# Optimization experiments

Hardware: AMD Instinct MI355X
Metric: run time of the kernel (lower is better)

## Reference

```python
import jax, jax.numpy as jnp
import numpy as np

N = 10000      # nodes
E = 160000     # edges
MUL = 64       # multiplicity of 0e and 1o in node feats / target
NATTR = 10     # number of element types (node_attrs one-hot width)
RDIM = 8       # radial (edge_feats) dim
NAVG = 16.0    # num_avg_neighbors
_INV3 = 0.5773502691896258  # CG coeff for 1o x 1o -> 0e (1/sqrt(3))


def setup_inputs() -> dict:
    key = jax.random.key(0)
    ks = jax.random.split(key, 20)
    return {
        "node_attrs": jax.random.uniform(ks[0], (N, NATTR), jnp.float32),
        "node_feats": jax.random.normal(ks[1], (N, 4 * MUL), jnp.float32),
        "edge_attrs_real": jax.random.normal(ks[2], (E, 4), jnp.float32),
        "edge_attrs_imag": jax.random.normal(ks[3], (E, 4), jnp.float32),
        "edge_feats": jax.random.normal(ks[4], (E, RDIM), jnp.float32),
        # linear_up (per-l internal weights)
        "W_up0": jax.random.normal(ks[5], (MUL, MUL), jnp.float32),
        "W_up1": jax.random.normal(ks[6], (MUL, MUL), jnp.float32),
        # conv_tp_weights MLP: [8, 64, 64, 64, 4*MUL]
        "M1": jax.random.normal(ks[7], (RDIM, 64), jnp.float32),
        "M2": jax.random.normal(ks[8], (64, 64), jnp.float32),
        "M3": jax.random.normal(ks[9], (64, 64), jnp.float32),
        "M4": jax.random.normal(ks[10], (64, 4 * MUL), jnp.float32),
        # linear: irreps_mid (128x0e+128x1o) -> irreps_nonlin (128x0e+64x1o)
        "W_lin_s": jax.random.normal(ks[11], (2 * MUL, 2 * MUL), jnp.float32),
        "W_lin_v": jax.random.normal(ks[12], (2 * MUL, MUL), jnp.float32),
        # skip_tp: FullyConnectedTensorProduct(node_feats, node_attrs -> irreps_nonlin)
        "W_sk_s": jax.random.normal(ks[13], (MUL, NATTR, 2 * MUL), jnp.float32),
        "W_sk_v": jax.random.normal(ks[14], (MUL, NATTR, MUL), jnp.float32),
        "edge_index": jax.random.randint(ks[15], (2, E), 0, N, jnp.int64
                                         if jax.config.jax_enable_x64 else jnp.int32),
    }


def _forward(node_attrs, node_feats, edge_attrs_real, edge_attrs_imag, edge_feats,
             W_up0, W_up1, M1, M2, M3, M4, W_lin_s, W_lin_v, W_sk_s, W_sk_v,
             sender, receiver):
    n = node_feats.shape[0]
    x0 = node_feats[:, :MUL]                          # (N, 64)   64x0e
    x1 = node_feats[:, MUL:].reshape(n, MUL, 3)       # (N, 64, 3) 64x1o

    # skip TP (fully connected, node_attrs are scalars)
    sk_norm = 1.0 / np.sqrt(MUL * NATTR)
    sc_s = jnp.einsum('nu,na,uav->nv', x0, node_attrs, W_sk_s) * sk_norm   # (N,128)
    sc_v = jnp.einsum('nui,na,uav->nvi', x1, node_attrs, W_sk_v) * sk_norm # (N,64,3)

    # linear_up (per-l)
    up_norm = 1.0 / np.sqrt(MUL)
    x0 = (x0 @ W_up0) * up_norm
    x1 = jnp.einsum('nui,uv->nvi', x1, W_up1) * up_norm

    # radial MLP -> per-edge TP weights (4 uvu paths x MUL)
    h = jax.nn.silu((edge_feats @ M1) / np.sqrt(RDIM))
    h = jax.nn.silu((h @ M2) / 8.0)
    h = jax.nn.silu((h @ M3) / 8.0)
    tw = (h @ M4) / 8.0                               # (E, 256)
    wA, wB, wC, wD = (tw[:, :MUL], tw[:, MUL:2*MUL],
                      tw[:, 2*MUL:3*MUL], tw[:, 3*MUL:])

    xs0 = x0[sender]                                  # (E, 64)
    xs1 = x1[sender]                                  # (E, 64, 3)

    def conv_tp(y):
        # y: (E,4) = [0e | 1o]; uvu paths with per-edge weights
        y0, y1 = y[:, :1], y[:, 1:]
        s = jnp.concatenate([xs0 * y0 * wA,                                  # 0e x 0e -> 0e
                             jnp.einsum('eui,ei->eu', xs1, y1) * _INV3 * wD  # 1o x 1o -> 0e
                             ], axis=1)                                      # (E,128)
        v = jnp.concatenate([(xs0 * wB)[:, :, None] * y1[:, None, :],        # 0e x 1o -> 1o
                             xs1 * (y0 * wC)[:, :, None]                     # 1o x 0e -> 1o
                             ], axis=1)                                      # (E,128,3)
        return s, v

    sr, vr = conv_tp(edge_attrs_real)
    si, vi = conv_tp(edge_attrs_imag)

    ms_r = jax.ops.segment_sum(sr, receiver, num_segments=n)
    mv_r = jax.ops.segment_sum(vr, receiver, num_segments=n)
    ms_i = jax.ops.segment_sum(si, receiver, num_segments=n)
    mv_i = jax.ops.segment_sum(vi, receiver, num_segments=n)

    lin_norm = (1.0 / np.sqrt(2 * MUL)) / (2.0 * NAVG)

    def lin(ms, mv):
        return (ms @ W_lin_s) * lin_norm, jnp.einsum('nui,uv->nvi', mv, W_lin_v) * lin_norm

    def gate(s, v):
        # irreps_nonlin = 64x0e scalars | 64x0e gates | 64x1o gated
        scal = jax.nn.silu(s[:, :MUL])
        g = jax.nn.silu(s[:, MUL:])
        return jnp.concatenate([scal, (v * g[:, :, None]).reshape(n, 3 * MUL)], axis=1)

    ls, lv = lin(ms_r, mv_r)
    real = gate(ls + sc_s, lv + sc_v)                 # (N, 256), residual on real part
    lsi, lvi = lin(ms_i, mv_i)
    imag = gate(lsi, lvi)                             # (N, 256)

    # view_as_complex + reshape [N, num_features, dim//num_features]; complex kept
    # as trailing real/imag axis of size 2.
    return jnp.stack([real, imag], axis=-1).reshape(n, MUL, (4 * MUL) // MUL, 2)


def reference(node_attrs, node_feats, edge_attrs_real, edge_attrs_imag, edge_feats,
              W_up0, W_up1, M1, M2, M3, M4, W_lin_s, W_lin_v, W_sk_s, W_sk_v,
              edge_index):
    sender, receiver = edge_index[0], edge_index[1]
    return _forward(node_attrs, node_feats, edge_attrs_real, edge_attrs_imag,
                    edge_feats, W_up0, W_up1, M1, M2, M3, M4,
                    W_lin_s, W_lin_v, W_sk_s, W_sk_v, sender, receiver)
```

## Files before the change

kernel.cpp:

```cpp
#include <hip/hip_runtime.h>
#include <hip/hip_bf16.h>

#define NN 10000
#define NE 160000
#define NGRP 625
#define XPLN 640000

#define SK_NORM   0.039528470752104741f
#define UP_NORM   0.125f
#define M1_NORM   0.35355339059327373f
#define INV3      0.5773502691896258f
#define LIN_NORM  0.0027621358640099516f

__device__ __forceinline__ float siluf(float x) { return x / (1.0f + __expf(-x)); }

__device__ __forceinline__ unsigned short f2bf_bits(float x) {
    union { __hip_bfloat16 h; unsigned short u; } cv;
    cv.h = __float2bfloat16(x);
    return cv.u;
}
__device__ __forceinline__ float bflo(unsigned int w) { return __uint_as_float(w << 16); }
__device__ __forceinline__ float bfhi(unsigned int w) { return __uint_as_float(w & 0xffff0000u); }

typedef short bf16x8 __attribute__((ext_vector_type(8)));
typedef float f32x4  __attribute__((ext_vector_type(4)));

__global__ __launch_bounds__(256) void k_detect(const int* __restrict__ ei32, int* __restrict__ flag) {
    __shared__ int cnt;
    if (threadIdx.x == 0) cnt = 0;
    __syncthreads();
    int z = 0;
    for (int i = threadIdx.x; i < 1024; i += 256)
        if (ei32[2 * i + 1] == 0) z++;
    atomicAdd(&cnt, z);
    __syncthreads();
    if (threadIdx.x == 0) flag[0] = (cnt >= 512) ? 1 : 0;
}

__global__ __launch_bounds__(256) void k_cvt(const int* __restrict__ ei32, const int* __restrict__ flag,
                                             int* __restrict__ snd, int* __restrict__ rcv) {
    int e = blockIdx.x * 256 + threadIdx.x;
    if (e >= NE) return;
    if (flag[0]) {
        const long long* e64 = (const long long*)ei32;
        snd[e] = (int)e64[e];
        rcv[e] = (int)e64[NE + e];
    } else {
        snd[e] = ei32[e];
        rcv[e] = ei32[NE + e];
    }
}

__global__ __launch_bounds__(256) void k_wprepN(
    const float* __restrict__ Wsk_s, const float* __restrict__ Wsk_v,
    const float* __restrict__ Wu0, const float* __restrict__ Wu1,
    unsigned short* __restrict__ WNF) {
    int idx = blockIdx.x * 256 + threadIdx.x;
    if (idx >= 131072) return;
    float val;
    if (idx < 81920) {
        int p = idx / 10240, r = idx % 10240;
        int kc = r >> 9, l8 = r & 511;
        int lane = l8 >> 3, j = l8 & 7, quad = lane >> 4, lo = lane & 15;
        int a = kc >> 1, u = (kc & 1) * 32 + quad * 8 + j;
        val = Wsk_s[(u * 10 + a) * 128 + p * 16 + lo];
    } else if (idx < 122880) {
        int rel = idx - 81920;
        int p = rel / 10240, r = rel % 10240;
        int kc = r >> 9, l8 = r & 511;
        int lane = l8 >> 3, j = l8 & 7, quad = lane >> 4, lo = lane & 15;
        int a = kc >> 1, u = (kc & 1) * 32 + quad * 8 + j;
        val = Wsk_v[(u * 10 + a) * 64 + p * 16 + lo];
    } else if (idx < 126976) {
        int rel = idx - 122880;
        int p = rel >> 10, r = rel & 1023;
        int kc = r >> 9, l8 = r & 511;
        int lane = l8 >> 3, j = l8 & 7, quad = lane >> 4, lo = lane & 15;
        int u = kc * 32 + quad * 8 + j;
        val = Wu0[u * 64 + p * 16 + lo];
    } else {
        int rel = idx - 126976;
        int p = rel >> 10, r = rel & 1023;
        int kc = r >> 9, l8 = r & 511;
        int lane = l8 >> 3, j = l8 & 7, quad = lane >> 4, lo = lane & 15;
        int u = kc * 32 + quad * 8 + j;
        val = Wu1[u * 64 + p * 16 + lo];
    }
    WNF[idx] = f2bf_bits(val);
}

__global__ __launch_bounds__(256) void k_xprep(
    const float* __restrict__ node_attrs, const float* __restrict__ node_feats,
    unsigned short* __restrict__ xpk, float* __restrict__ attrsP) {
    int idx = blockIdx.x * 256 + threadIdx.x;
    if (idx < 4 * NN * 64) {
        int n = idx >> 8, c = idx & 255;
        int plane = c >> 6, u = c & 63;
        float v = (plane == 0) ? node_feats[(long)n * 256 + u]
                               : node_feats[(long)n * 256 + 64 + u * 3 + (plane - 1)];
        xpk[(size_t)plane * XPLN + (long)n * 64 + u] = f2bf_bits(v);
        return;
    }
    int i2 = idx - 4 * NN * 64;
    if (i2 < 10 * NN) {
        int a = i2 / NN, n = i2 - a * NN;
        attrsP[i2] = node_attrs[(long)n * 10 + a];
    }
}

__global__ __launch_bounds__(256) void k_wprep2(
    const float* __restrict__ M1, const float* __restrict__ M2,
    const float* __restrict__ M3, const float* __restrict__ M4,
    unsigned short* __restrict__ WFG) {
    int idx = blockIdx.x * 256 + threadIdx.x;
    if (idx >= 52 * 512) return;
    int f = idx >> 9, r = idx & 511;
    int lane = r >> 3, j = r & 7;
    int quad = lane >> 4, lo = lane & 15;
    float val;
    if (f < 4) {
        int n = f * 16 + lo, k = quad * 8 + j;
        val = (k < 8) ? M1[k * 64 + n] : 0.f;
    } else if (f < 12) {
        int g2 = f - 4, nt = g2 >> 1, half = g2 & 1;
        int n = nt * 16 + lo, k = half * 32 + quad * 8 + j;
        val = M2[k * 64 + n];
    } else if (f < 20) {
        int g3 = f - 12, nt = g3 >> 1, half = g3 & 1;
        int n = nt * 16 + lo, k = half * 32 + quad * 8 + j;
        val = M3[k * 64 + n];
    } else {
        int g4 = f - 20, tt = g4 >> 1, half = g4 & 1;
        int n = tt * 16 + lo, k = half * 32 + quad * 8 + j;
        val = M4[k * 256 + n];
    }
    WFG[idx] = f2bf_bits(val);
}

#define G0 8
#define NB0 79
#define G2 4
#define NB2 157
#define G3 16
#define NB3 40
#define KNODE_GRID (4*NB0 + 2*NB2 + 2*NB3)

__global__ __launch_bounds__(128) void k_node(
    const unsigned short* __restrict__ xpk, const float* __restrict__ attrsP,
    const unsigned short* __restrict__ WNF,
    float* __restrict__ sc_s, float* __restrict__ sc_v,
    float* __restrict__ x0u, float* __restrict__ x1p) {
    __shared__ unsigned short pan[2 * 10240];
    __shared__ float att[10 * 128];

    int t = threadIdx.x;
    int bid = blockIdx.x;
    int type, vp, chunk;
    if (bid < 4 * NB0)                 { type = 0; vp = bid / NB0; chunk = bid % NB0; }
    else if (bid < 4 * NB0 + 2 * NB2)  { int r = bid - 4 * NB0; type = 2; vp = r / NB2; chunk = r % NB2; }
    else                               { int r = bid - 4 * NB0 - 2 * NB2; type = 3; vp = r / NB3; chunk = r % NB3; }
    int G = (type == 0) ? G0 : (type == 2 ? G2 : G3);
    int g0 = chunk * G;
    int ng = NGRP - g0; if (ng > G) ng = G;
    int n0 = g0 * 16;

    int psrc, pcnt;
    if (type == 0)      { psrc = vp * 2 * 10240;           pcnt = 20480; }
    else if (type == 2) { psrc = 81920 + vp * 2 * 10240;   pcnt = 20480; }
    else                { psrc = 122880 + vp * 2 * 1024;   pcnt = 2048;  }
    for (int i = t; i < pcnt / 8; i += 128)
        ((float4*)pan)[i] = ((const float4*)(WNF + psrc))[i];
    if (type == 3) {
        for (int i = t; i < 2048 / 8; i += 128)
            ((float4*)(pan + 2048))[i] = ((const float4*)(WNF + 126976 + vp * 2 * 1024))[i];
    }
    if (type <= 2) {
        int cnt = ng * 16;
        #pragma unroll
        for (int k = 0; k < 10; k++) {
            int i = k * 128 + t;
            int nl = t;
            if (nl < cnt) att[i] = attrsP[k * NN + n0 + nl];
        }
    }
    __syncthreads();

    int wv = t >> 6, lane = t & 63, lo = lane & 15, quad = lane >> 4;
    int lbase = lane * 8;
    const f32x4 zacc = {0.f, 0.f, 0.f, 0.f};
    const unsigned short* mypan = pan + wv * 10240;

    if (type == 0) {
        int vtg = vp * 2 + wv;
        const unsigned short* xb = xpk;
        bf16x8 nfa0 = *(const bf16x8*)(xb + (long)(n0 + lo) * 64 + quad * 8);
        bf16x8 nfa1 = *(const bf16x8*)(xb + (long)(n0 + lo) * 64 + 32 + quad * 8);
        #pragma unroll 1
        for (int g = 0; g < ng; g++) {
            bf16x8 fa0 = nfa0, fa1 = nfa1;
            if (g + 1 < ng) {
                nfa0 = *(const bf16x8*)(xb + (long)(n0 + (g + 1) * 16 + lo) * 64 + quad * 8);
                nfa1 = *(const bf16x8*)(xb + (long)(n0 + (g + 1) * 16 + lo) * 64 + 32 + quad * 8);
            }
            f32x4 acc = zacc;
            #pragma unroll
            for (int a = 0; a < 10; a++) {
                bf16x8 b0 = *(const bf16x8*)&mypan[(2 * a) * 512 + lbase];
                bf16x8 b1 = *(const bf16x8*)&mypan[(2 * a + 1) * 512 + lbase];
                f32x4 p = __builtin_amdgcn_mfma_f32_16x16x32_bf16(fa0, b0, zacc, 0, 0, 0);
                p = __builtin_amdgcn_mfma_f32_16x16x32_bf16(fa1, b1, p, 0, 0, 0);
                float4 afv = *(const float4*)&att[a * 128 + g * 16 + quad * 4];
                acc[0] += afv.x * p[0]; acc[1] += afv.y * p[1];
                acc[2] += afv.z * p[2]; acc[3] += afv.w * p[3];
            }
            int nb = n0 + g * 16;
            #pragma unroll
            for (int r = 0; r < 4; r++)
                sc_s[(long)(nb + quad * 4 + r) * 128 + vtg * 16 + lo] = acc[r] * SK_NORM;
        }
    } else if (type == 2) {
        int vt = vp * 2 + wv;
        bf16x8 nfa0[3], nfa1[3];
        #pragma unroll
        for (int i = 0; i < 3; i++) {
            const unsigned short* xb = xpk + (size_t)(1 + i) * XPLN + (long)(n0 + lo) * 64;
            nfa0[i] = *(const bf16x8*)(xb + quad * 8);
            nfa1[i] = *(const bf16x8*)(xb + 32 + quad * 8);
        }
        #pragma unroll 1
        for (int g = 0; g < ng; g++) {
            bf16x8 fa0[3], fa1[3];
            #pragma unroll
            for (int i = 0; i < 3; i++) { fa0[i] = nfa0[i]; fa1[i] = nfa1[i]; }
            if (g + 1 < ng) {
                #pragma unroll
                for (int i = 0; i < 3; i++) {
                    const unsigned short* xb = xpk + (size_t)(1 + i) * XPLN + (long)(n0 + (g + 1) * 16 + lo) * 64;
                    nfa0[i] = *(const bf16x8*)(xb + quad * 8);
                    nfa1[i] = *(const bf16x8*)(xb + 32 + quad * 8);
                }
            }
            f32x4 acc0 = zacc, acc1 = zacc, acc2 = zacc;
            #pragma unroll
            for (int a = 0; a < 10; a++) {
                bf16x8 b0 = *(const bf16x8*)&mypan[(2 * a) * 512 + lbase];
                bf16x8 b1 = *(const bf16x8*)&mypan[(2 * a + 1) * 512 + lbase];
                float4 afv = *(const float4*)&att[a * 128 + g * 16 + quad * 4];
                f32x4 p0 = __builtin_amdgcn_mfma_f32_16x16x32_bf16(fa0[0], b0, zacc, 0, 0, 0);
                p0 = __builtin_amdgcn_mfma_f32_16x16x32_bf16(fa1[0], b1, p0, 0, 0, 0);
                acc0[0] += afv.x * p0[0]; acc0[1] += afv.y * p0[1];
                acc0[2] += afv.z * p0[2]; acc0[3] += afv.w * p0[3];
                f32x4 p1 = __builtin_amdgcn_mfma_f32_16x16x32_bf16(fa0[1], b0, zacc, 0, 0, 0);
                p1 = __builtin_amdgcn_mfma_f32_16x16x32_bf16(fa1[1], b1, p1, 0, 0, 0);
                acc1[0] += afv.x * p1[0]; acc1[1] += afv.y * p1[1];
                acc1[2] += afv.z * p1[2]; acc1[3] += afv.w * p1[3];
                f32x4 p2 = __builtin_amdgcn_mfma_f32_16x16x32_bf16(fa0[2], b0, zacc, 0, 0, 0);
                p2 = __builtin_amdgcn_mfma_f32_16x16x32_bf16(fa1[2], b1, p2, 0, 0, 0);
                acc2[0] += afv.x * p2[0]; acc2[1] += afv.y * p2[1];
                acc2[2] += afv.z * p2[2]; acc2[3] += afv.w * p2[3];
            }
            int nb = n0 + g * 16;
            #pragma unroll
            for (int r = 0; r < 4; r++) {
                long rb = (long)(nb + quad * 4 + r) * 192 + vt * 16 + lo;
                sc_v[rb]       = acc0[r] * SK_NORM;
                sc_v[rb + 64]  = acc1[r] * SK_NORM;
                sc_v[rb + 128] = acc2[r] * SK_NORM;
            }
        }
    } else {
        int vt = vp * 2 + wv;
        bf16x8 bk20 = *(const bf16x8*)&pan[wv * 1024 + lbase];
        bf16x8 bk21 = *(const bf16x8*)&pan[wv * 1024 + 512 + lbase];
        bf16x8 bk30 = *(const bf16x8*)&pan[2048 + wv * 1024 + lbase];
        bf16x8 bk31 = *(const bf16x8*)&pan[2048 + wv * 1024 + 512 + lbase];
        #pragma unroll 1
        for (int g = 0; g < ng; g++) {
            int nb = n0 + g * 16;
            {
                const unsigned short* xb = xpk + (long)(nb + lo) * 64;
                bf16x8 fa0 = *(const bf16x8*)(xb + quad * 8);
                bf16x8 fa1 = *(const bf16x8*)(xb + 32 + quad * 8);
                f32x4 acc = __builtin_amdgcn_mfma_f32_16x16x32_bf16(fa0, bk20, zacc, 0, 0, 0);
                acc = __builtin_amdgcn_mfma_f32_16x16x32_bf16(fa1, bk21, acc, 0, 0, 0);
                #pragma unroll
                for (int r = 0; r < 4; r++)
                    x0u[(long)(nb + quad * 4 + r) * 64 + vt * 16 + lo] = acc[r] * UP_NORM;
            }
            #pragma unroll
            for (int i = 0; i < 3; i++) {
                const unsigned short* xb = xpk + (size_t)(1 + i) * XPLN + (long)(nb + lo) * 64;
                bf16x8 fa0 = *(const bf16x8*)(xb + quad * 8);
                bf16x8 fa1 = *(const bf16x8*)(xb + 32 + quad * 8);
                f32x4 acc = __builtin_amdgcn_mfma_f32_16x16x32_bf16(fa0, bk30, zacc, 0, 0, 0);
                acc = __builtin_amdgcn_mfma_f32_16x16x32_bf16(fa1, bk31, acc, 0, 0, 0);
                #pragma unroll
                for (int r = 0; r < 4; r++)
                    x1p[(size_t)i * XPLN + (long)(nb + quad * 4 + r) * 64 + vt * 16 + lo] = acc[r] * UP_NORM;
            }
        }
    }
}

__global__ __launch_bounds__(256) void k_hist(const int* __restrict__ rcv, int* __restrict__ counts) {
    int e = blockIdx.x * 256 + threadIdx.x;
    if (e < NE) atomicAdd(&counts[rcv[e]], 1);
}

__global__ __launch_bounds__(1024) void k_scan(const int* __restrict__ counts, int* __restrict__ offsets) {
    __shared__ int partial[1024];
    int t = threadIdx.x;
    const int CHUNK = (NN + 1023) / 1024;
    int base = t * CHUNK;
    int s = 0;
    for (int i = 0; i < CHUNK; i++) if (base + i < NN) s += counts[base + i];
    partial[t] = s;
    __syncthreads();
    for (int d = 1; d < 1024; d *= 2) {
        int v = (t >= d) ? partial[t - d] : 0;
        __syncthreads();
        partial[t] += v;
        __syncthreads();
    }
    int excl = (t == 0) ? 0 : partial[t - 1];
    for (int i = 0; i < CHUNK; i++) {
        if (base + i < NN) { offsets[base + i] = excl; excl += counts[base + i]; }
    }
    if (t == 1023) offsets[NN] = partial[1023];
}

__global__ __launch_bounds__(256) void k_fill(const int* __restrict__ rcv, const int* __restrict__ snd,
                                              const int* __restrict__ offsets,
                                              int* __restrict__ cursor, int2* __restrict__ epk) {
    int e = blockIdx.x * 256 + threadIdx.x;
    if (e < NE) {
        int r = rcv[e];
        int pos = atomicAdd(&cursor[r], 1);
        epk[offsets[r] + pos] = make_int2(snd[e], e);
    }
}

__global__ __launch_bounds__(256) void k_eprep(const int2* __restrict__ epk,
                                               const float4* __restrict__ ear, const float4* __restrict__ eai,
                                               const float4* __restrict__ ef,
                                               int* __restrict__ sndp,
                                               float4* __restrict__ earp, float4* __restrict__ eaip,
                                               float4* __restrict__ efp) {
    int j = blockIdx.x * 256 + threadIdx.x;
    if (j >= NE) return;
    int2 se = epk[j];
    sndp[j] = se.x;
    earp[j] = ear[se.y];
    eaip[j] = eai[se.y];
    efp[(long)j * 2]     = ef[(long)se.y * 2];
    efp[(long)j * 2 + 1] = ef[(long)se.y * 2 + 1];
}

#define HID_STRIDE 72
#define OB_STRIDE  40
#define EPB 128

__global__ __launch_bounds__(256) void k_edge_mlp(
    const float4* __restrict__ efp, const unsigned short* __restrict__ WFG,
    __hip_bfloat16* __restrict__ twp) {
    __shared__ unsigned short wfrag[52 * 512];
    __shared__ unsigned short hid[4][16 * HID_STRIDE];

    int t = threadIdx.x;
    for (int i = t; i < 52 * 512 / 8; i += 256)
        ((float4*)wfrag)[i] = ((const float4*)WFG)[i];
    __syncthreads();

    int wv = t >> 6;
    int lane = t & 63;
    int lo = lane & 15;
    int quad = lane >> 4;
    int lbase = lane * 8;
    unsigned short* myhid = hid[wv];
    unsigned short* myob  = hid[wv];
    const f32x4 zacc = {0.f, 0.f, 0.f, 0.f};

    #pragma unroll 1
    for (int g = 0; g < EPB / 64; g++) {
        int jbase = blockIdx.x * EPB + g * 64 + wv * 16;

        bf16x8 a1 = {0, 0, 0, 0, 0, 0, 0, 0};
        if (quad == 0) {
            float4 f0 = efp[(long)(jbase + lo) * 2];
            float4 f1 = efp[(long)(jbase + lo) * 2 + 1];
            union { unsigned short us[8]; bf16x8 v; } pk;
            pk.us[0] = f2bf_bits(f0.x * M1_NORM); pk.us[1] = f2bf_bits(f0.y * M1_NORM);
            pk.us[2] = f2bf_bits(f0.z * M1_NORM); pk.us[3] = f2bf_bits(f0.w * M1_NORM);
            pk.us[4] = f2bf_bits(f1.x * M1_NORM); pk.us[5] = f2bf_bits(f1.y * M1_NORM);
            pk.us[6] = f2bf_bits(f1.z * M1_NORM); pk.us[7] = f2bf_bits(f1.w * M1_NORM);
            a1 = pk.v;
        }
        {
            f32x4 acc[4];
            #pragma unroll
            for (int nt = 0; nt < 4; nt++) {
                bf16x8 b = *(const bf16x8*)&wfrag[nt * 512 + lbase];
                acc[nt] = __builtin_amdgcn_mfma_f32_16x16x32_bf16(a1, b, zacc, 0, 0, 0);
            }
            #pragma unroll
            for (int nt = 0; nt < 4; nt++)
                #pragma unroll
                for (int r = 0; r < 4; r++)
                    myhid[(quad * 4 + r) * HID_STRIDE + nt * 16 + lo] = f2bf_bits(siluf(acc[nt][r]));
        }

        #pragma unroll
        for (int L = 0; L < 2; L++) {
            int fb = 4 + L * 8;
            bf16x8 a0 = *(const bf16x8*)&myhid[lo * HID_STRIDE + quad * 8];
            bf16x8 a1v = *(const bf16x8*)&myhid[lo * HID_STRIDE + 32 + quad * 8];
            f32x4 acc[4];
            #pragma unroll
            for (int nt = 0; nt < 4; nt++) {
                bf16x8 b0 = *(const bf16x8*)&wfrag[(fb + nt * 2) * 512 + lbase];
                bf16x8 b1 = *(const bf16x8*)&wfrag[(fb + nt * 2 + 1) * 512 + lbase];
                acc[nt] = __builtin_amdgcn_mfma_f32_16x16x32_bf16(a0, b0, zacc, 0, 0, 0);
                acc[nt] = __builtin_amdgcn_mfma_f32_16x16x32_bf16(a1v, b1, acc[nt], 0, 0, 0);
            }
            #pragma unroll
            for (int nt = 0; nt < 4; nt++)
                #pragma unroll
                for (int r = 0; r < 4; r++)
                    myhid[(quad * 4 + r) * HID_STRIDE + nt * 16 + lo] = f2bf_bits(siluf(acc[nt][r] * 0.125f));
        }

        {
            bf16x8 a0 = *(const bf16x8*)&myhid[lo * HID_STRIDE + quad * 8];
            bf16x8 a1v = *(const bf16x8*)&myhid[lo * HID_STRIDE + 32 + quad * 8];
            int sedge = lane >> 2, sch = lane & 3;
            #pragma unroll 1
            for (int rd = 0; rd < 8; rd++) {
                f32x4 acc2[2];
                #pragma unroll
                for (int p = 0; p < 2; p++) {
                    int tt = (rd < 4) ? (p * 4 + rd) : (8 + p * 4 + (rd - 4));
                    bf16x8 b0 = *(const bf16x8*)&wfrag[(20 + tt * 2) * 512 + lbase];
                    bf16x8 b1 = *(const bf16x8*)&wfrag[(20 + tt * 2 + 1) * 512 + lbase];
                    acc2[p] = __builtin_amdgcn_mfma_f32_16x16x32_bf16(a0, b0, zacc, 0, 0, 0);
                    acc2[p] = __builtin_amdgcn_mfma_f32_16x16x32_bf16(a1v, b1, acc2[p], 0, 0, 0);
                }
                #pragma unroll
                for (int p = 0; p < 2; p++)
                    #pragma unroll
                    for (int r = 0; r < 4; r++)
                        myob[(quad * 4 + r) * OB_STRIDE + 2 * lo + p] = f2bf_bits(acc2[p][r] * 0.125f);
                bf16x8 vv = *(const bf16x8*)&myob[sedge * OB_STRIDE + sch * 8];
                *(bf16x8*)(twp + (long)(jbase + sedge) * 256 + rd * 32 + sch * 8) = vv;
            }
        }
    }
}

#define CB2 4
__global__ __launch_bounds__(256) void k_conv(
    const int* __restrict__ offsets, const int* __restrict__ sndp,
    const float4* __restrict__ earp, const float4* __restrict__ eaip,
    const float* __restrict__ x0u, const float* __restrict__ x1p,
    const __hip_bfloat16* __restrict__ twp,
    unsigned short* __restrict__ msgbuf) {
    __shared__ float red[2 * 64 * 9];
    int n = blockIdx.x;
    int t = threadIdx.x;
    int wv = t >> 6;
    int u = t & 63;
    int path = wv >> 1;
    int wpar = wv & 1;
    int beg = offsets[n], end = offsets[n + 1];
    float a0r = 0.f, a1r = 0.f, a2r = 0.f, a3r = 0.f;
    float a0i = 0.f, a1i = 0.f, a2i = 0.f, a3i = 0.f;
    if (path == 0) {
        const int tsel = 2 * u;
        for (int jb = beg + wpar * CB2; jb < end; jb += 2 * CB2) {
            unsigned int twd[CB2]; float x0v[CB2]; float4 yr[CB2], yi[CB2];
            #pragma unroll
            for (int p = 0; p < CB2; p++) {
                int j = jb + p;
                int jc = (j < end) ? j : (end - 1);
                int s = sndp[jc];
                yr[p] = earp[jc];
                yi[p] = eaip[jc];
                x0v[p] = x0u[(long)s * 64 + u];
                twd[p] = (j < end) ? *(const unsigned int*)(twp + (long)jc * 256 + tsel) : 0u;
            }
            #pragma unroll
            for (int p = 0; p < CB2; p++) {
                float wA = bflo(twd[p]), wB = bfhi(twd[p]);
                float xa = x0v[p] * wA, xb = x0v[p] * wB;
                a0r += xa * yr[p].x; a1r += xb * yr[p].y; a2r += xb * yr[p].z; a3r += xb * yr[p].w;
                a0i += xa * yi[p].x; a1i += xb * yi[p].y; a2i += xb * yi[p].z; a3i += xb * yi[p].w;
            }
        }
    } else {
        const int tsel = 128 + 2 * u;
        for (int jb = beg + wpar * CB2; jb < end; jb += 2 * CB2) {
            unsigned int twd[CB2]; float xv0[CB2], xv1[CB2], xv2[CB2]; float4 yr[CB2], yi[CB2];
            #pragma unroll
            for (int p = 0; p < CB2; p++) {
                int j = jb + p;
                int jc = (j < end) ? j : (end - 1);
                int s = sndp[jc];
                yr[p] = earp[jc];
                yi[p] = eaip[jc];
                long sb = (long)s * 64 + u;
                xv0[p] = x1p[sb];
                xv1[p] = x1p[XPLN + sb];
                xv2[p] = x1p[2 * XPLN + sb];
                twd[p] = (j < end) ? *(const unsigned int*)(twp + (long)jc * 256 + tsel) : 0u;
            }
            #pragma unroll
            for (int p = 0; p < CB2; p++) {
                float wC = bflo(twd[p]), wDs = bfhi(twd[p]) * INV3;
                float dr = xv0[p] * yr[p].y + xv1[p] * yr[p].z + xv2[p] * yr[p].w;
                float di = xv0[p] * yi[p].y + xv1[p] * yi[p].z + xv2[p] * yi[p].w;
                a0r += dr * wDs; a0i += di * wDs;
                float ycr = yr[p].x * wC, yci = yi[p].x * wC;
                a1r += xv0[p] * ycr; a2r += xv1[p] * ycr; a3r += xv2[p] * ycr;
                a1i += xv0[p] * yci; a2i += xv1[p] * yci; a3i += xv2[p] * yci;
            }
        }
    }
    float* rb = &red[(path * 64 + u) * 9];
    if (wpar == 1) {
        rb[0] = a0r; rb[1] = a1r; rb[2] = a2r; rb[3] = a3r;
        rb[4] = a0i; rb[5] = a1i; rb[6] = a2i; rb[7] = a3i;
    }
    __syncthreads();
    if (wpar == 0) {
        a0r += rb[0]; a1r += rb[1]; a2r += rb[2]; a3r += rb[3];
        a0i += rb[4]; a1i += rb[5]; a2i += rb[6]; a3i += rb[7];
        unsigned short* mb = msgbuf + (long)n * 1024;
        int off = path * 64 + u;
        mb[off]       = f2bf_bits(a0r);
        mb[128 + off] = f2bf_bits(a0i);
        mb[256 + off]             = f2bf_bits(a1r);
        mb[256 + 128 + off]       = f2bf_bits(a2r);
        mb[256 + 256 + off]       = f2bf_bits(a3r);
        mb[256 + 384 + off]       = f2bf_bits(a1i);
        mb[256 + 384 + 128 + off] = f2bf_bits(a2i);
        mb[256 + 384 + 256 + off] = f2bf_bits(a3i);
    }
}

#define WL_STRIDE 136
#define SV_STRIDE 129
#define VV_STRIDE 65

__global__ __launch_bounds__(256) void k_lin(
    const unsigned short* __restrict__ msgbuf,
    const float* __restrict__ sc_s, const float* __restrict__ sc_v,
    const float* __restrict__ W_lin_s, const float* __restrict__ W_lin_v,
    float* __restrict__ out) {
    __shared__ unsigned short wst[128 * WL_STRIDE];
    __shared__ unsigned short wvt[64 * WL_STRIDE];
    __shared__ float sval[2 * 16 * SV_STRIDE];
    __shared__ float vval[2 * 3 * 16 * VV_STRIDE];

    int t = threadIdx.x;
    for (int idx = t; idx < 128 * 128; idx += 256) {
        int k = idx >> 7, v = idx & 127;
        wst[v * WL_STRIDE + k] = f2bf_bits(W_lin_s[idx]);
    }
    for (int idx = t; idx < 128 * 64; idx += 256) {
        int k = idx >> 6, v = idx & 63;
        wvt[v * WL_STRIDE + k] = f2bf_bits(W_lin_v[idx]);
    }
    __syncthreads();

    int wv = t >> 6;
    int lane = t & 63;
    int lo = lane & 15;
    int quad = lane >> 4;
    const f32x4 zacc = {0.f, 0.f, 0.f, 0.f};

    for (int g = blockIdx.x; g < NN / 16; g += gridDim.x) {
        long nbase = (long)g * 16;
        const unsigned short* arow = msgbuf + (nbase + lo) * 1024;

        #pragma unroll 1
        for (int q = 0; q < 10; q++) {
            int tau = wv + q * 4;
            int aoff, cidx, cstride;
            const unsigned short* bptr;
            float* cbuf;
            if (tau < 16) {
                int ri = tau >> 3, vt = tau & 7;
                aoff = ri * 128;
                bptr = &wst[(vt * 16 + lo) * WL_STRIDE];
                cbuf = sval;
                cidx = (ri * 16) * SV_STRIDE + vt * 16 + lo;
                cstride = SV_STRIDE;
            } else {
                int tp = tau - 16;
                int ri = tp / 12, rem = tp % 12;
                int i = rem >> 2, vt = rem & 3;
                aoff = 256 + ri * 384 + i * 128;
                bptr = &wvt[(vt * 16 + lo) * WL_STRIDE];
                cbuf = vval;
                cidx = ((ri * 3 + i) * 16) * VV_STRIDE + vt * 16 + lo;
                cstride = VV_STRIDE;
            }
            f32x4 acc = zacc;
            #pragma unroll
            for (int ks = 0; ks < 4; ks++) {
                bf16x8 a = *(const bf16x8*)(arow + aoff + ks * 32 + quad * 8);
                bf16x8 b = *(const bf16x8*)(bptr + ks * 32 + quad * 8);
                acc = __builtin_amdgcn_mfma_f32_16x16x32_bf16(a, b, acc, 0, 0, 0);
            }
            #pragma unroll
            for (int r = 0; r < 4; r++)
                cbuf[cidx + (quad * 4 + r) * cstride] = acc[r] * LIN_NORM;
        }
        __syncthreads();

        #pragma unroll 1
        for (int j = 0; j < 16; j++) {
            int c = t;
            long gn = nbase + j;
            float re, im;
            if (c < 64) {
                float sr = sval[(0 * 16 + j) * SV_STRIDE + c] + sc_s[gn * 128 + c];
                float si = sval[(1 * 16 + j) * SV_STRIDE + c];
                re = siluf(sr); im = siluf(si);
            } else {
                int rem = c - 64;
                int v = rem / 3;
                int i = rem - v * 3;
                float gr = siluf(sval[(0 * 16 + j) * SV_STRIDE + 64 + v] + sc_s[gn * 128 + 64 + v]);
                float gi = siluf(sval[(1 * 16 + j) * SV_STRIDE + 64 + v]);
                float lr = vval[((0 * 3 + i) * 16 + j) * VV_STRIDE + v] + sc_v[gn * 192 + i * 64 + v];
                float li = vval[((1 * 3 + i) * 16 + j) * VV_STRIDE + v];
                re = lr * gr; im = li * gi;
            }
            ((float2*)out)[gn * 256 + c] = make_float2(re, im);
        }
        __syncthreads();
    }
}

extern "C" void kernel_launch(void* const* d_in, const int* in_sizes, int n_in,
                              void* d_out, int out_size, void* d_ws, size_t ws_size,
                              hipStream_t stream) {
    const float* node_attrs = (const float*)d_in[0];
    const float* node_feats = (const float*)d_in[1];
    const float* ear        = (const float*)d_in[2];
    const float* eai        = (const float*)d_in[3];
    const float* edge_feats = (const float*)d_in[4];
    const float* W_up0      = (const float*)d_in[5];
    const float* W_up1      = (const float*)d_in[6];
    const float* M1         = (const float*)d_in[7];
    const float* M2         = (const float*)d_in[8];
    const float* M3         = (const float*)d_in[9];
    const float* M4         = (const float*)d_in[10];
    const float* W_lin_s    = (const float*)d_in[11];
    const float* W_lin_v    = (const float*)d_in[12];
    const float* W_sk_s     = (const float*)d_in[13];
    const float* W_sk_v     = (const float*)d_in[14];
    const int*   ei         = (const int*)d_in[15];

    char* ws = (char*)d_ws;
    size_t o_x0u = 0;
    size_t o_x1p = o_x0u + (size_t)NN * 64 * 4;
    size_t o_scs = o_x1p + (size_t)NN * 256 * 4;
    size_t o_scv = o_scs + (size_t)NN * 128 * 4;
    size_t o_tw  = o_scv + (size_t)NN * 192 * 4;
    size_t o_cnt = o_tw  + (size_t)NE * 256 * 2;
    size_t o_cur = o_cnt + (size_t)NN * 4;
    size_t o_ofs = o_cur + (size_t)NN * 4;
    size_t o_epk = o_ofs + (size_t)(NN + 1) * 4 + 60;
    size_t o_snd = o_epk + (size_t)NE * 8;
    size_t o_rcv = o_snd + (size_t)NE * 4;
    size_t o_flg = o_rcv + (size_t)NE * 4;
    size_t o_msg = o_flg + 64;
    size_t o_wnf = o_msg + (size_t)NN * 1024 * 2;
    size_t o_snp = o_wnf + 262144;
    size_t o_erp = o_snp + (size_t)NE * 4;
    size_t o_eip = o_erp + (size_t)NE * 16;
    size_t o_efp = o_eip + (size_t)NE * 16;
    size_t o_wfg = o_efp + (size_t)NE * 32;
    size_t o_xpk = o_wfg + (size_t)52 * 512 * 2;
    size_t o_atp = o_xpk + (size_t)4 * NN * 64 * 2;

    float* x0u = (float*)(ws + o_x0u);
    float* x1p = (float*)(ws + o_x1p);
    float* sc_s = (float*)(ws + o_scs);
    float* sc_v = (float*)(ws + o_scv);
    __hip_bfloat16* twp = (__hip_bfloat16*)(ws + o_tw);
    int* counts  = (int*)(ws + o_cnt);
    int* cursor  = (int*)(ws + o_cur);
    int* offsets = (int*)(ws + o_ofs);
    int2* epk    = (int2*)(ws + o_epk);
    int* snd     = (int*)(ws + o_snd);
    int* rcv     = (int*)(ws + o_rcv);
    int* flag    = (int*)(ws + o_flg);
    unsigned short* msgbuf = (unsigned short*)(ws + o_msg);
    unsigned short* WNF = (unsigned short*)(ws + o_wnf);
    int*    sndp = (int*)(ws + o_snp);
    float4* earp = (float4*)(ws + o_erp);
    float4* eaip = (float4*)(ws + o_eip);
    float4* efp  = (float4*)(ws + o_efp);
    unsigned short* WFG = (unsigned short*)(ws + o_wfg);
    unsigned short* xpk = (unsigned short*)(ws + o_xpk);
    float* attrsP = (float*)(ws + o_atp);

    hipMemsetAsync(ws + o_cnt, 0, (size_t)NN * 8, stream);

    dim3 b256(256), b1024(1024), b128(128);
    k_detect<<<dim3(1), b256, 0, stream>>>(ei, flag);
    k_cvt   <<<dim3((NE + 255) / 256), b256, 0, stream>>>(ei, flag, snd, rcv);
    k_hist<<<dim3((NE + 255) / 256), b256, 0, stream>>>(rcv, counts);
    k_scan<<<dim3(1), b1024, 0, stream>>>(counts, offsets);
    k_fill<<<dim3((NE + 255) / 256), b256, 0, stream>>>(rcv, snd, offsets, cursor, epk);
    k_eprep<<<dim3((NE + 255) / 256), b256, 0, stream>>>(epk, (const float4*)ear, (const float4*)eai,
                                                         (const float4*)edge_feats,
                                                         sndp, earp, eaip, efp);
    k_wprepN<<<dim3(512), b256, 0, stream>>>(W_sk_s, W_sk_v, W_up0, W_up1, WNF);
    k_wprep2<<<dim3(104), b256, 0, stream>>>(M1, M2, M3, M4, WFG);
    k_xprep <<<dim3((4 * NN * 64 + 10 * NN + 255) / 256), b256, 0, stream>>>(node_attrs, node_feats, xpk, attrsP);
    k_node  <<<dim3(KNODE_GRID), b128, 0, stream>>>(xpk, attrsP, WNF, sc_s, sc_v, x0u, x1p);
    k_edge_mlp<<<dim3(NE / EPB), b256, 0, stream>>>(efp, WFG, twp);
    k_conv<<<dim3(NN), b256, 0, stream>>>(offsets, sndp, earp, eaip, x0u, x1p, twp, msgbuf);
    k_lin <<<dim3(224), b256, 0, stream>>>(msgbuf, sc_s, sc_v, W_lin_s, W_lin_v, (float*)d_out);
}
```

Baseline: 300.1 us.

## Pre-pack linear weights and messages into MFMA fragment layout, one group per block

Measured after the change: 276.9 us. 1.08x faster.

```diff
diff --git a/kernel.cpp b/kernel.cpp
--- a/kernel.cpp
+++ b/kernel.cpp
@@ -111,30 +111,48 @@
 __global__ __launch_bounds__(256) void k_wprep2(
     const float* __restrict__ M1, const float* __restrict__ M2,
     const float* __restrict__ M3, const float* __restrict__ M4,
-    unsigned short* __restrict__ WFG) {
+    const float* __restrict__ W_lin_s, const float* __restrict__ W_lin_v,
+    unsigned short* __restrict__ WFG, unsigned short* __restrict__ WLF) {
     int idx = blockIdx.x * 256 + threadIdx.x;
-    if (idx >= 52 * 512) return;
-    int f = idx >> 9, r = idx & 511;
-    int lane = r >> 3, j = r & 7;
-    int quad = lane >> 4, lo = lane & 15;
-    float val;
-    if (f < 4) {
-        int n = f * 16 + lo, k = quad * 8 + j;
-        val = (k < 8) ? M1[k * 64 + n] : 0.f;
-    } else if (f < 12) {
-        int g2 = f - 4, nt = g2 >> 1, half = g2 & 1;
-        int n = nt * 16 + lo, k = half * 32 + quad * 8 + j;
-        val = M2[k * 64 + n];
-    } else if (f < 20) {
-        int g3 = f - 12, nt = g3 >> 1, half = g3 & 1;
-        int n = nt * 16 + lo, k = half * 32 + quad * 8 + j;
-        val = M3[k * 64 + n];
+    if (idx >= (52 + 48) * 512) return;
+    if (idx < 52 * 512) {
+        int f = idx >> 9, r = idx & 511;
+        int lane = r >> 3, j = r & 7;
+        int quad = lane >> 4, lo = lane & 15;
+        float val;
+        if (f < 4) {
+            int n = f * 16 + lo, k = quad * 8 + j;
+            val = (k < 8) ? M1[k * 64 + n] : 0.f;
+        } else if (f < 12) {
+            int g2 = f - 4, nt = g2 >> 1, half = g2 & 1;
+            int n = nt * 16 + lo, k = half * 32 + quad * 8 + j;
+            val = M2[k * 64 + n];
+        } else if (f < 20) {
+            int g3 = f - 12, nt = g3 >> 1, half = g3 & 1;
+            int n = nt * 16 + lo, k = half * 32 + quad * 8 + j;
+            val = M3[k * 64 + n];
+        } else {
+            int g4 = f - 20, tt = g4 >> 1, half = g4 & 1;
+            int n = tt * 16 + lo, k = half * 32 + quad * 8 + j;
+            val = M4[k * 256 + n];
+        }
+        WFG[idx] = f2bf_bits(val);
     } else {
-        int g4 = f - 20, tt = g4 >> 1, half = g4 & 1;
-        int n = tt * 16 + lo, k = half * 32 + quad * 8 + j;
-        val = M4[k * 256 + n];
-    }
-    WFG[idx] = f2bf_bits(val);
+        int rel = idx - 52 * 512;
+        int f = rel >> 9, r = rel & 511;
+        int lane = r >> 3, j = r & 7;
+        int quad = lane >> 4, lo = lane & 15;
+        float val;
+        if (f < 32) {
+            int vt = f >> 2, ks = f & 3;
+            val = W_lin_s[(ks * 32 + quad * 8 + j) * 128 + vt * 16 + lo];
+        } else {
+            int f2 = f - 32;
+            int vt = f2 >> 2, ks = f2 & 3;
+            val = W_lin_v[(ks * 32 + quad * 8 + j) * 64 + vt * 16 + lo];
+        }
+        WLF[rel] = f2bf_bits(val);
+    }
 }
 
 #define G0 8
@@ -462,8 +480,9 @@
     const float4* __restrict__ earp, const float4* __restrict__ eaip,
     const float* __restrict__ x0u, const float* __restrict__ x1p,
     const __hip_bfloat16* __restrict__ twp,
-    unsigned short* __restrict__ msgbuf) {
+    unsigned short* __restrict__ msgF) {
     __shared__ float red[2 * 64 * 9];
+    __shared__ unsigned short stg[1024];
     int n = blockIdx.x;
     int t = threadIdx.x;
     int wv = t >> 6;
@@ -533,112 +552,120 @@
     if (wpar == 0) {
         a0r += rb[0]; a1r += rb[1]; a2r += rb[2]; a3r += rb[3];
         a0i += rb[4]; a1i += rb[5]; a2i += rb[6]; a3i += rb[7];
-        unsigned short* mb = msgbuf + (long)n * 1024;
-        int off = path * 64 + u;
-        mb[off]       = f2bf_bits(a0r);
-        mb[128 + off] = f2bf_bits(a0i);
-        mb[256 + off]             = f2bf_bits(a1r);
-        mb[256 + 128 + off]       = f2bf_bits(a2r);
-        mb[256 + 256 + off]       = f2bf_bits(a3r);
-        mb[256 + 384 + off]       = f2bf_bits(a1i);
-        mb[256 + 384 + 128 + off] = f2bf_bits(a2i);
-        mb[256 + 384 + 256 + off] = f2bf_bits(a3i);
-    }
-}
-
-#define WL_STRIDE 136
+        int cu = path * 64 + u;
+        stg[cu]       = f2bf_bits(a0r);
+        stg[128 + cu] = f2bf_bits(a0i);
+        stg[256 + cu] = f2bf_bits(a1r);
+        stg[384 + cu] = f2bf_bits(a2r);
+        stg[512 + cu] = f2bf_bits(a3r);
+        stg[640 + cu] = f2bf_bits(a1i);
+        stg[768 + cu] = f2bf_bits(a2i);
+        stg[896 + cu] = f2bf_bits(a3i);
+    }
+    __syncthreads();
+    if (t < 128) {
+        int g = n >> 4, lo = n & 15;
+        bf16x8 vv = *(const bf16x8*)&stg[t * 8];
+        *(bf16x8*)(msgF + (size_t)g * 16384 + (t >> 2) * 512 + lo * 32 + (t & 3) * 8) = vv;
+    }
+}
+
 #define SV_STRIDE 129
 #define VV_STRIDE 65
 
-__global__ __launch_bounds__(256) void k_lin(
-    const unsigned short* __restrict__ msgbuf,
+__global__ __launch_bounds__(256, 3) void k_lin(
+    const unsigned short* __restrict__ msgF,
     const float* __restrict__ sc_s, const float* __restrict__ sc_v,
-    const float* __restrict__ W_lin_s, const float* __restrict__ W_lin_v,
+    const unsigned short* __restrict__ WLF,
     float* __restrict__ out) {
-    __shared__ unsigned short wst[128 * WL_STRIDE];
-    __shared__ unsigned short wvt[64 * WL_STRIDE];
-    __shared__ float sval[2 * 16 * SV_STRIDE];
-    __shared__ float vval[2 * 3 * 16 * VV_STRIDE];
+    __shared__ char smem[49152];
+    unsigned short* wfrag = (unsigned short*)smem;
+    float* sval = (float*)smem;
+    float* vval = (float*)(smem + 2 * 16 * SV_STRIDE * 4);
 
     int t = threadIdx.x;
-    for (int idx = t; idx < 128 * 128; idx += 256) {
-        int k = idx >> 7, v = idx & 127;
-        wst[v * WL_STRIDE + k] = f2bf_bits(W_lin_s[idx]);
-    }
-    for (int idx = t; idx < 128 * 64; idx += 256) {
-        int k = idx >> 6, v = idx & 63;
-        wvt[v * WL_STRIDE + k] = f2bf_bits(W_lin_v[idx]);
-    }
+    for (int i = t; i < 48 * 512 / 8; i += 256)
+        ((float4*)wfrag)[i] = ((const float4*)WLF)[i];
     __syncthreads();
 
     int wv = t >> 6;
     int lane = t & 63;
     int lo = lane & 15;
     int quad = lane >> 4;
+    int lbase = lane * 8;
+    int aoff_lane = lo * 32 + quad * 8;
     const f32x4 zacc = {0.f, 0.f, 0.f, 0.f};
 
-    for (int g = blockIdx.x; g < NN / 16; g += gridDim.x) {
-        long nbase = (long)g * 16;
-        const unsigned short* arow = msgbuf + (nbase + lo) * 1024;
-
-        #pragma unroll 1
-        for (int q = 0; q < 10; q++) {
-            int tau = wv + q * 4;
-            int aoff, cidx, cstride;
-            const unsigned short* bptr;
-            float* cbuf;
-            if (tau < 16) {
-                int ri = tau >> 3, vt = tau & 7;
-                aoff = ri * 128;
-                bptr = &wst[(vt * 16 + lo) * WL_STRIDE];
-                cbuf = sval;
-                cidx = (ri * 16) * SV_STRIDE + vt * 16 + lo;
-                cstride = SV_STRIDE;
-            } else {
-                int tp = tau - 16;
-                int ri = tp / 12, rem = tp % 12;
-                int i = rem >> 2, vt = rem & 3;
-                aoff = 256 + ri * 384 + i * 128;
-                bptr = &wvt[(vt * 16 + lo) * WL_STRIDE];
-                cbuf = vval;
-                cidx = ((ri * 3 + i) * 16) * VV_STRIDE + vt * 16 + lo;
-                cstride = VV_STRIDE;
-            }
-            f32x4 acc = zacc;
-            #pragma unroll
-            for (int ks = 0; ks < 4; ks++) {
-                bf16x8 a = *(const bf16x8*)(arow + aoff + ks * 32 + quad * 8);
-                bf16x8 b = *(const bf16x8*)(bptr + ks * 32 + quad * 8);
-                acc = __builtin_amdgcn_mfma_f32_16x16x32_bf16(a, b, acc, 0, 0, 0);
-            }
+    long g = blockIdx.x;
+    long nbase = g * 16;
+    const unsigned short* agbase = msgF + (size_t)g * 16384;
+
+    f32x4 accs[10];
+    #pragma unroll
+    for (int q = 0; q < 10; q++) {
+        int tau = wv + q * 4;
+        int cblk, fb;
+        if (tau < 16) {
+            int ri = tau >> 3, vt = tau & 7;
+            cblk = ri; fb = vt * 4;
+        } else {
+            int tp = tau - 16;
+            int ri = tp / 12, rem = tp % 12;
+            int i = rem >> 2, vt = rem & 3;
+            cblk = 2 + ri * 3 + i; fb = 32 + vt * 4;
+        }
+        f32x4 acc = zacc;
+        #pragma unroll
+        for (int ks = 0; ks < 4; ks++) {
+            bf16x8 a = *(const bf16x8*)(agbase + (cblk * 4 + ks) * 512 + aoff_lane);
+            bf16x8 b = *(const bf16x8*)&wfrag[(fb + ks) * 512 + lbase];
+            acc = __builtin_amdgcn_mfma_f32_16x16x32_bf16(a, b, acc, 0, 0, 0);
+        }
+        accs[q] = acc;
+    }
+    __syncthreads();
+
+    #pragma unroll
+    for (int q = 0; q < 10; q++) {
+        int tau = wv + q * 4;
+        if (tau < 16) {
+            int ri = tau >> 3, vt = tau & 7;
+            int cidx = (ri * 16) * SV_STRIDE + vt * 16 + lo;
             #pragma unroll
             for (int r = 0; r < 4; r++)
-                cbuf[cidx + (quad * 4 + r) * cstride] = acc[r] * LIN_NORM;
-        }
-        __syncthreads();
-
-        #pragma unroll 1
-        for (int j = 0; j < 16; j++) {
-            int c = t;
-            long gn = nbase + j;
-            float re, im;
-            if (c < 64) {
-                float sr = sval[(0 * 16 + j) * SV_STRIDE + c] + sc_s[gn * 128 + c];
-                float si = sval[(1 * 16 + j) * SV_STRIDE + c];
-                re = siluf(sr); im = siluf(si);
-            } else {
-                int rem = c - 64;
-                int v = rem / 3;
-                int i = rem - v * 3;
-                float gr = siluf(sval[(0 * 16 + j) * SV_STRIDE + 64 + v] + sc_s[gn * 128 + 64 + v]);
-                float gi = siluf(sval[(1 * 16 + j) * SV_STRIDE + 64 + v]);
-                float lr = vval[((0 * 3 + i) * 16 + j) * VV_STRIDE + v] + sc_v[gn * 192 + i * 64 + v];
-                float li = vval[((1 * 3 + i) * 16 + j) * VV_STRIDE + v];
-                re = lr * gr; im = li * gi;
-            }
-            ((float2*)out)[gn * 256 + c] = make_float2(re, im);
-        }
-        __syncthreads();
+                sval[cidx + (quad * 4 + r) * SV_STRIDE] = accs[q][r] * LIN_NORM;
+        } else {
+            int tp = tau - 16;
+            int ri = tp / 12, rem = tp % 12;
+            int i = rem >> 2, vt = rem & 3;
+            int cidx = ((ri * 3 + i) * 16) * VV_STRIDE + vt * 16 + lo;
+            #pragma unroll
+            for (int r = 0; r < 4; r++)
+                vval[cidx + (quad * 4 + r) * VV_STRIDE] = accs[q][r] * LIN_NORM;
+        }
+    }
+    __syncthreads();
+
+    #pragma unroll 1
+    for (int j = 0; j < 16; j++) {
+        int c = t;
+        long gn = nbase + j;
+        float re, im;
+        if (c < 64) {
+            float sr = sval[(0 * 16 + j) * SV_STRIDE + c] + sc_s[gn * 128 + c];
+            float si = sval[(1 * 16 + j) * SV_STRIDE + c];
+            re = siluf(sr); im = siluf(si);
+        } else {
+            int rem = c - 64;
+            int v = rem / 3;
+            int i = rem - v * 3;
+            float gr = siluf(sval[(0 * 16 + j) * SV_STRIDE + 64 + v] + sc_s[gn * 128 + 64 + v]);
+            float gi = siluf(sval[(1 * 16 + j) * SV_STRIDE + 64 + v]);
+            float lr = vval[((0 * 3 + i) * 16 + j) * VV_STRIDE + v] + sc_v[gn * 192 + i * 64 + v];
+            float li = vval[((1 * 3 + i) * 16 + j) * VV_STRIDE + v];
+            re = lr * gr; im = li * gi;
+        }
+        ((float2*)out)[gn * 256 + c] = make_float2(re, im);
     }
 }
 
@@ -682,7 +709,8 @@
     size_t o_eip = o_erp + (size_t)NE * 16;
     size_t o_efp = o_eip + (size_t)NE * 16;
     size_t o_wfg = o_efp + (size_t)NE * 32;
-    size_t o_xpk = o_wfg + (size_t)52 * 512 * 2;
+    size_t o_wlf = o_wfg + (size_t)52 * 512 * 2;
+    size_t o_xpk = o_wlf + (size_t)48 * 512 * 2;
     size_t o_atp = o_xpk + (size_t)4 * NN * 64 * 2;
 
     float* x0u = (float*)(ws + o_x0u);
@@ -697,13 +725,14 @@
     int* snd     = (int*)(ws + o_snd);
     int* rcv     = (int*)(ws + o_rcv);
     int* flag    = (int*)(ws + o_flg);
-    unsigned short* msgbuf = (unsigned short*)(ws + o_msg);
+    unsigned short* msgF = (unsigned short*)(ws + o_msg);
     unsigned short* WNF = (unsigned short*)(ws + o_wnf);
     int*    sndp = (int*)(ws + o_snp);
     float4* earp = (float4*)(ws + o_erp);
     float4* eaip = (float4*)(ws + o_eip);
     float4* efp  = (float4*)(ws + o_efp);
     unsigned short* WFG = (unsigned short*)(ws + o_wfg);
+    unsigned short* WLF = (unsigned short*)(ws + o_wlf);
     unsigned short* xpk = (unsigned short*)(ws + o_xpk);
     float* attrsP = (float*)(ws + o_atp);
 
@@ -719,10 +748,10 @@
                                                          (const float4*)edge_feats,
                                                          sndp, earp, eaip, efp);
     k_wprepN<<<dim3(512), b256, 0, stream>>>(W_sk_s, W_sk_v, W_up0, W_up1, WNF);
-    k_wprep2<<<dim3(104), b256, 0, stream>>>(M1, M2, M3, M4, WFG);
+    k_wprep2<<<dim3(200), b256, 0, stream>>>(M1, M2, M3, M4, W_lin_s, W_lin_v, WFG, WLF);
     k_xprep <<<dim3((4 * NN * 64 + 10 * NN + 255) / 256), b256, 0, stream>>>(node_attrs, node_feats, xpk, attrsP);
     k_node  <<<dim3(KNODE_GRID), b128, 0, stream>>>(xpk, attrsP, WNF, sc_s, sc_v, x0u, x1p);
     k_edge_mlp<<<dim3(NE / EPB), b256, 0, stream>>>(efp, WFG, twp);
-    k_conv<<<dim3(NN), b256, 0, stream>>>(offsets, sndp, earp, eaip, x0u, x1p, twp, msgbuf);
-    k_lin <<<dim3(224), b256, 0, stream>>>(msgbuf, sc_s, sc_v, W_lin_s, W_lin_v, (float*)d_out);
-}
+    k_conv<<<dim3(NN), b256, 0, stream>>>(offsets, sndp, earp, eaip, x0u, x1p, twp, msgF);
+    k_lin <<<dim3(NGRP), b256, 0, stream>>>(msgF, sc_s, sc_v, WLF, (float*)d_out);
+}
```
